# Kernel tuning notes

Measured on AMD Instinct MI355X. Metric: run time of the kernel, lower is better.

## Reference

```python
import jax, jax.numpy as jnp
import numpy as np

M = 32000   # query points
N = 32000   # support points
H = 32      # neighbors per query
C = 64      # channels
K = 15      # kernel points (shell_sizes=[1,14])
GROUPS = 8
CH_PER_GRP = C // GROUPS   # 8
COUT = K * CH_PER_GRP      # 120
RADIUS = 2.5
SIGMA = 1.0
INF = 1.0e6


def _leaky_relu(x):
    return jnp.where(x >= 0, x, 0.1 * x)


def setup_inputs() -> dict:
    key = jax.random.key(0)
    ks = jax.random.split(key, 9)
    q_pts = jax.random.normal(ks[0], (M, 3), jnp.float32) * RADIUS
    s_pts = jax.random.normal(ks[1], (N, 3), jnp.float32) * RADIUS
    s_feats = jax.random.normal(ks[2], (N, C), jnp.float32)
    neighb_inds = jax.random.randint(ks[3], (M, H), 0, N)
    # kernel points in a sphere of given radius, first point fixed at center
    kp = jax.random.normal(ks[4], (K, 3), jnp.float32)
    kp = kp / (jnp.linalg.norm(kp, axis=1, keepdims=True) + 1e-9)
    r = RADIUS * jax.random.uniform(ks[5], (K, 1), jnp.float32) ** (1.0 / 3.0)
    kp = kp * r
    kernel_points = kp.at[0].set(0.0)
    # kaiming-uniform-ish conv weights (K, C)
    bound = 1.0 / np.sqrt(C)
    weights = jax.random.uniform(ks[6], (K, C), jnp.float32, -bound, bound)
    # alpha_mlp: Linear(C,C) + LeakyReLU(0.1) + Linear(C,Cout, no bias)
    w1 = jax.random.normal(ks[7], (C, C), jnp.float32) * (1.0 / np.sqrt(C))
    b1 = jnp.zeros((C,), jnp.float32)
    w2 = jax.random.normal(ks[8], (C, COUT), jnp.float32) * (1.0 / np.sqrt(C))
    return {"q_pts": q_pts, "s_pts": s_pts, "s_feats": s_feats,
            "neighb_inds": neighb_inds, "kernel_points": kernel_points,
            "weights": weights, "w1": w1, "b1": b1, "w2": w2}


def reference(q_pts, s_pts, s_feats, neighb_inds, kernel_points, weights, w1, b1, w2):
    # --- gather neighbor features (padded with a zero row) ---
    padded_feats = jnp.concatenate([s_feats, jnp.zeros((1, C), s_feats.dtype)], axis=0)
    neighbor_feats = padded_feats[neighb_inds]                      # (M, H, C)

    # --- attention modulations (M == N branch: pooled_feats = s_feats) ---
    pooled_feats = s_feats                                           # (M, C)
    mod = _leaky_relu(pooled_feats @ w1 + b1) @ w2                   # (M, Cout)
    mod = jax.nn.sigmoid(mod).reshape(M, K, CH_PER_GRP, 1)
    conv_w = weights.reshape(1, K, CH_PER_GRP, GROUPS) * mod         # (M, K, cpg, g)
    conv_w = conv_w.reshape(M, K, C)

    # --- kernel-point influences (no-grad in original) ---
    s_pts_pad = jnp.concatenate([s_pts, jnp.full((1, 3), INF, s_pts.dtype)], axis=0)
    neighbors = s_pts_pad[neighb_inds] - q_pts[:, None, :]           # (M, H, 3)
    diff = neighbors[:, :, None, :] - kernel_points[None, None, :, :]  # (M, H, K, 3)
    sq_d = jnp.sum(diff * diff, axis=-1)                             # (M, H, K)
    nn_sq = jnp.min(sq_d, axis=2)                                    # (M, H)
    nn_idx = jnp.argmin(sq_d, axis=2)                                # (M, H)
    infl = jnp.clip(1.0 - jnp.sqrt(nn_sq) / SIGMA, 0.0)              # linear influence
    infl = jax.lax.stop_gradient(infl)

    # --- gather per-neighbor kernel weights, modulate and aggregate ---
    nw = jnp.take_along_axis(conv_w, nn_idx[:, :, None], axis=1)     # (M, H, C)
    nw = nw * infl[:, :, None]
    return jnp.sum(neighbor_feats * nw, axis=1)                      # (M, C)
```

## Files before the change

kernel.cpp:

```cpp
#include <hip/hip_runtime.h>


#define MQ 32000

typedef unsigned short u16;
typedef unsigned int   u32;
typedef __attribute__((ext_vector_type(8))) short bf16x8;
typedef __attribute__((ext_vector_type(4))) float f32x4;

__device__ __forceinline__ float rlf(float v, int l) {
    return __int_as_float(__builtin_amdgcn_readlane(__float_as_int(v), l));
}
__device__ __forceinline__ int rli(int v, int l) {
    return __builtin_amdgcn_readlane(v, l);
}
__device__ __forceinline__ u16 f2bf(float x) {
    u32 u = __float_as_uint(x);
    return (u16)((u + 0x7FFFu + ((u >> 16) & 1u)) >> 16);
}
__device__ __forceinline__ float bf2f(u16 b) {
    return __uint_as_float(((u32)b) << 16);
}

__global__ __launch_bounds__(256, 2)
void mod_mlp_mfma(const float* __restrict__ s_feats,
                  const float* __restrict__ w1,
                  const float* __restrict__ b1,
                  const float* __restrict__ w2,
                  float* __restrict__ modw,
                  u16*   __restrict__ fb)
{
    __shared__ u16 w1b[64 * 64];
    __shared__ u16 w2b[64 * 128];
    __shared__ u16 hb[4][16 * 64];

    const int tid = threadIdx.x;
    for (int i = tid; i < 64 * 64; i += 256) w1b[i] = f2bf(w1[i]);
    for (int i = tid; i < 64 * 128; i += 256) {
        int k = i >> 7, j = i & 127;
        w2b[i] = (j < 120) ? f2bf(w2[k * 120 + j]) : (u16)0;
    }
    __syncthreads();

    const int lane = tid & 63;
    const int wid  = tid >> 6;
    const int jj   = lane & 15;
    const int rb   = (lane >> 4) * 8;
    const int rowC = (lane >> 4) * 4;

    bf16x8 b1f[4][2];
    #pragma unroll
    for (int nt = 0; nt < 4; ++nt)
        #pragma unroll
        for (int kk = 0; kk < 2; ++kk)
            #pragma unroll
            for (int r = 0; r < 8; ++r)
                b1f[nt][kk][r] = (short)w1b[(kk * 32 + rb + r) * 64 + nt * 16 + jj];

    bf16x8 b2f[8][2];
    #pragma unroll
    for (int nt = 0; nt < 8; ++nt)
        #pragma unroll
        for (int kk = 0; kk < 2; ++kk)
            #pragma unroll
            for (int r = 0; r < 8; ++r)
                b2f[nt][kk][r] = (short)w2b[(kk * 32 + rb + r) * 128 + nt * 16 + jj];

    float b1v[4];
    #pragma unroll
    for (int nt = 0; nt < 4; ++nt) b1v[nt] = b1[nt * 16 + jj];

    u16* hrow = &hb[wid][0];
    const int t = blockIdx.x * 4 + wid;
    const int m0 = t * 16;

    const float* ar = s_feats + (size_t)(m0 + jj) * 64 + rb;
    float4 v0 = *(const float4*)(ar);
    float4 v1 = *(const float4*)(ar + 4);
    float4 v2 = *(const float4*)(ar + 32);
    float4 v3 = *(const float4*)(ar + 36);
    bf16x8 a0, a1;
    a0[0] = (short)f2bf(v0.x); a0[1] = (short)f2bf(v0.y);
    a0[2] = (short)f2bf(v0.z); a0[3] = (short)f2bf(v0.w);
    a0[4] = (short)f2bf(v1.x); a0[5] = (short)f2bf(v1.y);
    a0[6] = (short)f2bf(v1.z); a0[7] = (short)f2bf(v1.w);
    a1[0] = (short)f2bf(v2.x); a1[1] = (short)f2bf(v2.y);
    a1[2] = (short)f2bf(v2.z); a1[3] = (short)f2bf(v2.w);
    a1[4] = (short)f2bf(v3.x); a1[5] = (short)f2bf(v3.y);
    a1[6] = (short)f2bf(v3.z); a1[7] = (short)f2bf(v3.w);

    *(bf16x8*)(fb + (size_t)(m0 + jj) * 64 + rb)      = a0;
    *(bf16x8*)(fb + (size_t)(m0 + jj) * 64 + 32 + rb) = a1;

    f32x4 acc[4];
    #pragma unroll
    for (int nt = 0; nt < 4; ++nt) {
        f32x4 z = {0.f, 0.f, 0.f, 0.f};
        z = __builtin_amdgcn_mfma_f32_16x16x32_bf16(a0, b1f[nt][0], z, 0, 0, 0);
        acc[nt] = __builtin_amdgcn_mfma_f32_16x16x32_bf16(a1, b1f[nt][1], z, 0, 0, 0);
    }
    #pragma unroll
    for (int nt = 0; nt < 4; ++nt) {
        #pragma unroll
        for (int r = 0; r < 4; ++r) {
            float h = acc[nt][r] + b1v[nt];
            h = (h >= 0.f) ? h : 0.1f * h;
            hrow[(rowC + r) * 64 + nt * 16 + jj] = f2bf(h);
        }
    }
    bf16x8 ha0 = *(bf16x8*)(hrow + jj * 64 + rb);
    bf16x8 ha1 = *(bf16x8*)(hrow + jj * 64 + 32 + rb);

    #pragma unroll
    for (int nt = 0; nt < 8; ++nt) {
        f32x4 z = {0.f, 0.f, 0.f, 0.f};
        z = __builtin_amdgcn_mfma_f32_16x16x32_bf16(ha0, b2f[nt][0], z, 0, 0, 0);
        f32x4 c2 = __builtin_amdgcn_mfma_f32_16x16x32_bf16(ha1, b2f[nt][1], z, 0, 0, 0);
        const int j = nt * 16 + jj;
        if (j < 120) {
            #pragma unroll
            for (int r = 0; r < 4; ++r)
                modw[(size_t)(m0 + rowC + r) * 120 + j] = 1.f / (1.f + __expf(-c2[r]));
        }
    }
}

__global__ __launch_bounds__(256, 4)
void kp_gather_v3(const float* __restrict__ q_pts,
                  const float* __restrict__ s_pts,
                  const u16*   __restrict__ fb,
                  const int*   __restrict__ neighb_inds,
                  const float* __restrict__ kpts,
                  const float* __restrict__ weights,
                  const float* __restrict__ modw,
                  float* __restrict__ out)
{
    __shared__ float wt_lds[15 * 64];
    const int tid = threadIdx.x;
    if (tid < 240) ((float4*)wt_lds)[tid] = ((const float4*)weights)[tid];
    __syncthreads();

    const int lane = tid & 63;
    const int wid  = tid >> 6;
    const int pair = blockIdx.x * 4 + wid;
    const int m0 = pair * 2;

    const int ind = __builtin_nontemporal_load(&neighb_inds[(size_t)m0 * 32 + lane]);

    const int cdiv = lane & 7;
    const int hl   = lane >> 3;
    bf16x8 fv[2][4];
    #pragma unroll
    for (int qq = 0; qq < 2; ++qq)
        #pragma unroll
        for (int cc = 0; cc < 4; ++cc) {
            const int ih = __shfl(ind, qq * 32 + cc * 8 + hl);
            fv[qq][cc] = *(const bf16x8*)(fb + (size_t)(u32)ih * 64 + cdiv * 8);
        }

    const size_t mb0 = (size_t)m0 * 120, mb1 = mb0 + 120;
    const float vA0 = __builtin_nontemporal_load(&modw[mb0 + lane]);
    const float vB0 = (lane < 56) ? __builtin_nontemporal_load(&modw[mb0 + 64 + lane]) : 0.f;
    const float vA1 = __builtin_nontemporal_load(&modw[mb1 + lane]);
    const float vB1 = (lane < 56) ? __builtin_nontemporal_load(&modw[mb1 + 64 + lane]) : 0.f;

    const int q = lane >> 5;
    const int m = m0 + q;
    const float qx = q_pts[m * 3 + 0];
    const float qy = q_pts[m * 3 + 1];
    const float qz = q_pts[m * 3 + 2];
    const float px = s_pts[(size_t)ind * 3 + 0] - qx;
    const float py = s_pts[(size_t)ind * 3 + 1] - qy;
    const float pz = s_pts[(size_t)ind * 3 + 2] - qz;
    float best = 1e30f; int bk = 0;
    #pragma unroll
    for (int k = 0; k < 15; ++k) {
        float ex = px - kpts[k * 3 + 0];
        float ey = py - kpts[k * 3 + 1];
        float ez = pz - kpts[k * 3 + 2];
        float d2 = fmaf(ex, ex, fmaf(ey, ey, ez * ez));
        if (d2 < best) { best = d2; bk = k; }
    }
    const float infl = fmaxf(0.f, 1.f - sqrtf(best));

    float acc[2][8];
    #pragma unroll
    for (int qq = 0; qq < 2; ++qq)
        #pragma unroll
        for (int e = 0; e < 8; ++e) acc[qq][e] = 0.f;

    #pragma unroll
    for (int qq = 0; qq < 2; ++qq) {
        #pragma unroll
        for (int cc = 0; cc < 4; ++cc) {
            const int idx = qq * 32 + cc * 8 + hl;
            const int kh  = __shfl(bk, idx);
            const float fl = __shfl(infl, idx);
            const int j = kh * 8 + cdiv;
            const float svA = __shfl(qq ? vA1 : vA0, j & 63);
            const float svB = __shfl(qq ? vB1 : vB0, (j - 64) & 63);
            const float w = ((j < 64) ? svA : svB) * fl;
            const float4 wa = *(const float4*)&wt_lds[kh * 64 + cdiv * 8];
            const float4 wb = *(const float4*)&wt_lds[kh * 64 + cdiv * 8 + 4];
            const bf16x8 f8 = fv[qq][cc];
            acc[qq][0] = fmaf(bf2f((u16)f8[0]), wa.x * w, acc[qq][0]);
            acc[qq][1] = fmaf(bf2f((u16)f8[1]), wa.y * w, acc[qq][1]);
            acc[qq][2] = fmaf(bf2f((u16)f8[2]), wa.z * w, acc[qq][2]);
            acc[qq][3] = fmaf(bf2f((u16)f8[3]), wa.w * w, acc[qq][3]);
            acc[qq][4] = fmaf(bf2f((u16)f8[4]), wb.x * w, acc[qq][4]);
            acc[qq][5] = fmaf(bf2f((u16)f8[5]), wb.y * w, acc[qq][5]);
            acc[qq][6] = fmaf(bf2f((u16)f8[6]), wb.z * w, acc[qq][6]);
            acc[qq][7] = fmaf(bf2f((u16)f8[7]), wb.w * w, acc[qq][7]);
        }
    }

    #pragma unroll
    for (int step = 8; step <= 32; step <<= 1)
        #pragma unroll
        for (int qq = 0; qq < 2; ++qq)
            #pragma unroll
            for (int e = 0; e < 8; ++e)
                acc[qq][e] += __shfl_xor(acc[qq][e], step);

    if (hl == 0) {
        #pragma unroll
        for (int qq = 0; qq < 2; ++qq) {
            f32x4 o0 = {acc[qq][0], acc[qq][1], acc[qq][2], acc[qq][3]};
            f32x4 o1 = {acc[qq][4], acc[qq][5], acc[qq][6], acc[qq][7]};
            float* dst = out + (size_t)(m0 + qq) * 64 + cdiv * 8;
            __builtin_nontemporal_store(o0, (f32x4*)dst);
            __builtin_nontemporal_store(o1, (f32x4*)(dst + 4));
        }
    }
}

__global__ __launch_bounds__(256, 3)
void mod_mlp(const float* __restrict__ s_feats,
             const float* __restrict__ w1,
             const float* __restrict__ b1,
             const float* __restrict__ w2,
             float* __restrict__ modw)
{
    __shared__ float w1_lds[64 * 64];
    __shared__ float w2_lds[64 * 120 + 8];

    const int tid = threadIdx.x;
    {
        const float4* s1 = (const float4*)w1;
        float4* d1 = (float4*)w1_lds;
        #pragma unroll
        for (int i = 0; i < 4; ++i) d1[tid + 256 * i] = s1[tid + 256 * i];
        const float4* s2 = (const float4*)w2;
        float4* d2 = (float4*)w2_lds;
        for (int i = tid; i < (64 * 120) / 4; i += 256) d2[i] = s2[i];
        if (tid < 8) w2_lds[64 * 120 + tid] = 0.f;
    }
    __syncthreads();

    const int lane = tid & 63;
    const int wid  = tid >> 6;
    const int c    = lane;
    const int nwaves = gridDim.x * 4;
    const int gwave  = blockIdx.x * 4 + wid;
    const float b1v = b1[c];
    const int cB = 64 + ((c < 56) ? c : 55);

    for (int pair = gwave; pair * 2 < MQ; pair += nwaves) {
        const int m0 = pair * 2;
        float f0 = s_feats[(size_t)m0 * 64 + c];
        float f1 = s_feats[(size_t)(m0 + 1) * 64 + c];
        float h0a = b1v, h0b = 0.f, h1a = b1v, h1b = 0.f;
        #pragma unroll
        for (int i = 0; i < 64; i += 2) {
            float wa = w1_lds[i * 64 + c];
            float wb = w1_lds[(i + 1) * 64 + c];
            h0a = fmaf(rlf(f0, i), wa, h0a);
            h0b = fmaf(rlf(f0, i + 1), wb, h0b);
            h1a = fmaf(rlf(f1, i), wa, h1a);
            h1b = fmaf(rlf(f1, i + 1), wb, h1b);
        }
        float h0 = h0a + h0b, h1 = h1a + h1b;
        h0 = (h0 >= 0.f) ? h0 : 0.1f * h0;
        h1 = (h1 >= 0.f) ? h1 : 0.1f * h1;
        float a00 = 0.f, a01 = 0.f, a10 = 0.f, a11 = 0.f;
        #pragma unroll
        for (int i = 0; i < 64; ++i) {
            float wA = w2_lds[i * 120 + c];
            float wB = w2_lds[i * 120 + cB];
            float s0 = rlf(h0, i);
            float s1 = rlf(h1, i);
            a00 = fmaf(s0, wA, a00);
            a01 = fmaf(s0, wB, a01);
            a10 = fmaf(s1, wA, a10);
            a11 = fmaf(s1, wB, a11);
        }
        modw[(size_t)m0 * 120 + c]       = 1.f / (1.f + __expf(-a00));
        modw[(size_t)(m0 + 1) * 120 + c] = 1.f / (1.f + __expf(-a10));
        if (c < 56) {
            modw[(size_t)m0 * 120 + 64 + c]       = 1.f / (1.f + __expf(-a01));
            modw[(size_t)(m0 + 1) * 120 + 64 + c] = 1.f / (1.f + __expf(-a11));
        }
    }
}

__global__ __launch_bounds__(256, 4)
void kp_gather(const float* __restrict__ q_pts,
               const float* __restrict__ s_pts,
               const float* __restrict__ s_feats,
               const int*   __restrict__ neighb_inds,
               const float* __restrict__ kpts,
               const float* __restrict__ weights,
               const float* __restrict__ modw,
               float* __restrict__ out)
{
    __shared__ float wt_lds[15 * 64];
    const int tid = threadIdx.x;
    if (tid < 240) ((float4*)wt_lds)[tid] = ((const float4*)weights)[tid];
    __syncthreads();

    const int lane = tid & 63;
    const int wid  = tid >> 6;
    const int c    = lane;
    const int u    = c >> 3;
    const int pair = blockIdx.x * 4 + wid;
    const int m0 = pair * 2;

    const int q = lane >> 5;
    const int m = m0 + q;
    const int ind = neighb_inds[(size_t)m0 * 32 + lane];
    const float qx = q_pts[m * 3 + 0];
    const float qy = q_pts[m * 3 + 1];
    const float qz = q_pts[m * 3 + 2];
    const float px = s_pts[(size_t)ind * 3 + 0] - qx;
    const float py = s_pts[(size_t)ind * 3 + 1] - qy;
    const float pz = s_pts[(size_t)ind * 3 + 2] - qz;
    float best = 1e30f; int bk = 0;
    #pragma unroll
    for (int k = 0; k < 15; ++k) {
        float ex = px - kpts[k * 3 + 0];
        float ey = py - kpts[k * 3 + 1];
        float ez = pz - kpts[k * 3 + 2];
        float d2 = fmaf(ex, ex, fmaf(ey, ey, ez * ez));
        if (d2 < best) { best = d2; bk = k; }
    }
    const float infl = fmaxf(0.f, 1.f - sqrtf(best));
    const int pk = (ind << 4) | bk;

    const size_t mb0 = (size_t)m0 * 120, mb1 = mb0 + 120;
    const float vA0 = modw[mb0 + c];
    const float vB0 = (c < 56) ? modw[mb0 + 64 + c] : 0.f;
    const float vA1 = modw[mb1 + c];
    const float vB1 = (c < 56) ? modw[mb1 + 64 + c] : 0.f;

    float fv0[32], fv1[32];
    #pragma unroll
    for (int h = 0; h < 32; ++h)
        fv0[h] = s_feats[(size_t)(rli(pk, h) >> 4) * 64 + c];
    #pragma unroll
    for (int h = 0; h < 32; ++h)
        fv1[h] = s_feats[(size_t)(rli(pk, 32 + h) >> 4) * 64 + c];

    float p0 = 0.f, p1 = 0.f, p2 = 0.f, p3 = 0.f;
    #pragma unroll
    for (int h = 0; h < 32; h += 4) {
        #pragma unroll
        for (int j = 0; j < 4; ++j) {
            const int s = rli(pk, h + j);
            const int kh = s & 15;
            const float fl = rlf(infl, h + j);
            const float sv = (kh < 8) ? __shfl(vA0, (kh << 3) + u)
                                      : __shfl(vB0, ((kh - 8) << 3) + u);
            const float w = wt_lds[(kh << 6) + c] * sv * fl;
            float& p = (j == 0) ? p0 : (j == 1) ? p1 : (j == 2) ? p2 : p3;
            p = fmaf(fv0[h + j], w, p);
        }
    }
    const float acc0 = (p0 + p1) + (p2 + p3);

    float r0 = 0.f, r1 = 0.f, r2 = 0.f, r3 = 0.f;
    #pragma unroll
    for (int h = 0; h < 32; h += 4) {
        #pragma unroll
        for (int j = 0; j < 4; ++j) {
            const int s = rli(pk, 32 + h + j);
            const int kh = s & 15;
            const float fl = rlf(infl, 32 + h + j);
            const float sv = (kh < 8) ? __shfl(vA1, (kh << 3) + u)
                                      : __shfl(vB1, ((kh - 8) << 3) + u);
            const float w = wt_lds[(kh << 6) + c] * sv * fl;
            float& p = (j == 0) ? r0 : (j == 1) ? r1 : (j == 2) ? r2 : r3;
            p = fmaf(fv1[h + j], w, p);
        }
    }
    const float acc1 = (r0 + r1) + (r2 + r3);

    out[(size_t)m0 * 64 + c]       = acc0;
    out[(size_t)(m0 + 1) * 64 + c] = acc1;
}

extern "C" void kernel_launch(void* const* d_in, const int* in_sizes, int n_in,
                              void* d_out, int out_size, void* d_ws, size_t ws_size,
                              hipStream_t stream) {
    const float* q_pts       = (const float*)d_in[0];
    const float* s_pts       = (const float*)d_in[1];
    const float* s_feats     = (const float*)d_in[2];
    const int*   neighb_inds = (const int*)d_in[3];
    const float* kpts        = (const float*)d_in[4];
    const float* weights     = (const float*)d_in[5];
    const float* w1          = (const float*)d_in[6];
    const float* b1          = (const float*)d_in[7];
    const float* w2          = (const float*)d_in[8];
    float* out = (float*)d_out;

    const size_t needFB   = (size_t)MQ * 64 * sizeof(u16);
    const size_t needMODW = (size_t)MQ * 120 * sizeof(float);
    if (ws_size >= needFB + needMODW) {
        u16*   fb   = (u16*)d_ws;
        float* modw = (float*)((char*)d_ws + needFB);
        mod_mlp_mfma<<<500, 256, 0, stream>>>(s_feats, w1, b1, w2, modw, fb);
        kp_gather_v3<<<MQ / 8, 256, 0, stream>>>(q_pts, s_pts, fb, neighb_inds,
                                                 kpts, weights, modw, out);
    } else {
        float* modw = (float*)d_ws;
        mod_mlp<<<768, 256, 0, stream>>>(s_feats, w1, b1, w2, modw);
        kp_gather<<<MQ / 8, 256, 0, stream>>>(q_pts, s_pts, s_feats, neighb_inds,
                                              kpts, weights, modw, out);
    }
}
```

Measured before the change: 116.9 us.

## Store modulation weights as bf16 and pre-pack MLP weight fragments in a prep kernel

Adds a one-block prep kernel that converts w1/w2 to bf16 in MFMA fragment order, so each MLP block loads its B fragments directly instead of converting through LDS with a barrier. The sigmoid modulation tensor is written as bf16 and read as packed 32-bit pairs in the gather kernel, halving that intermediate's write and read traffic. This costs an extra kernel launch and lowers modulation precision to bf16.

```diff
diff --git a/kernel.cpp b/kernel.cpp
--- a/kernel.cpp
+++ b/kernel.cpp
@@ -22,56 +22,45 @@
     return __uint_as_float(((u32)b) << 16);
 }
 
+__global__ void prep_weights(const float* __restrict__ w1,
+                             const float* __restrict__ w2,
+                             u16* __restrict__ w1p,
+                             u16* __restrict__ w2p)
+{
+    const int tid = threadIdx.x;
+    for (int i = tid; i < 64 * 64; i += 256) {
+        const int k = i >> 6, j = i & 63;
+        const int dst = (((k >> 5) * 4 + ((k >> 3) & 3)) * 4 + (j >> 4)) * 128
+                        + (j & 15) * 8 + (k & 7);
+        w1p[dst] = f2bf(w1[i]);
+    }
+    for (int i = tid; i < 64 * 128; i += 256) {
+        const int k = i >> 7, j = i & 127;
+        const int dst = (((k >> 5) * 4 + ((k >> 3) & 3)) * 8 + (j >> 4)) * 128
+                        + (j & 15) * 8 + (k & 7);
+        w2p[dst] = (j < 120) ? f2bf(w2[k * 120 + j]) : (u16)0;
+    }
+}
+
 __global__ __launch_bounds__(256, 2)
-void mod_mlp_mfma(const float* __restrict__ s_feats,
-                  const float* __restrict__ w1,
-                  const float* __restrict__ b1,
-                  const float* __restrict__ w2,
-                  float* __restrict__ modw,
-                  u16*   __restrict__ fb)
+void mod_mlp_mfma2(const float* __restrict__ s_feats,
+                   const u16*   __restrict__ w1p,
+                   const float* __restrict__ b1,
+                   const u16*   __restrict__ w2p,
+                   u16* __restrict__ modw,
+                   u16* __restrict__ fb)
 {
-    __shared__ u16 w1b[64 * 64];
-    __shared__ u16 w2b[64 * 128];
     __shared__ u16 hb[4][16 * 64];
 
-    const int tid = threadIdx.x;
-    for (int i = tid; i < 64 * 64; i += 256) w1b[i] = f2bf(w1[i]);
-    for (int i = tid; i < 64 * 128; i += 256) {
-        int k = i >> 7, j = i & 127;
-        w2b[i] = (j < 120) ? f2bf(w2[k * 120 + j]) : (u16)0;
-    }
-    __syncthreads();
-
+    const int tid  = threadIdx.x;
     const int lane = tid & 63;
     const int wid  = tid >> 6;
     const int jj   = lane & 15;
-    const int rb   = (lane >> 4) * 8;
-    const int rowC = (lane >> 4) * 4;
-
-    bf16x8 b1f[4][2];
-    #pragma unroll
-    for (int nt = 0; nt < 4; ++nt)
-        #pragma unroll
-        for (int kk = 0; kk < 2; ++kk)
-            #pragma unroll
-            for (int r = 0; r < 8; ++r)
-                b1f[nt][kk][r] = (short)w1b[(kk * 32 + rb + r) * 64 + nt * 16 + jj];
-
-    bf16x8 b2f[8][2];
-    #pragma unroll
-    for (int nt = 0; nt < 8; ++nt)
-        #pragma unroll
-        for (int kk = 0; kk < 2; ++kk)
-            #pragma unroll
-            for (int r = 0; r < 8; ++r)
-                b2f[nt][kk][r] = (short)w2b[(kk * 32 + rb + r) * 128 + nt * 16 + jj];
-
-    float b1v[4];
-    #pragma unroll
-    for (int nt = 0; nt < 4; ++nt) b1v[nt] = b1[nt * 16 + jj];
-
-    u16* hrow = &hb[wid][0];
-    const int t = blockIdx.x * 4 + wid;
+    const int rbg  = lane >> 4;
+    const int rb   = rbg * 8;
+    const int rowC = rbg * 4;
+
+    const int t  = blockIdx.x * 4 + wid;
     const int m0 = t * 16;
 
     const float* ar = s_feats + (size_t)(m0 + jj) * 64 + rb;
@@ -92,13 +81,20 @@
     *(bf16x8*)(fb + (size_t)(m0 + jj) * 64 + rb)      = a0;
     *(bf16x8*)(fb + (size_t)(m0 + jj) * 64 + 32 + rb) = a1;
 
+    float b1v[4];
+    #pragma unroll
+    for (int nt = 0; nt < 4; ++nt) b1v[nt] = b1[nt * 16 + jj];
+
     f32x4 acc[4];
     #pragma unroll
     for (int nt = 0; nt < 4; ++nt) {
+        const bf16x8 f0 = *(const bf16x8*)(w1p + ((0 * 4 + rbg) * 4 + nt) * 128 + jj * 8);
+        const bf16x8 f1 = *(const bf16x8*)(w1p + ((1 * 4 + rbg) * 4 + nt) * 128 + jj * 8);
         f32x4 z = {0.f, 0.f, 0.f, 0.f};
-        z = __builtin_amdgcn_mfma_f32_16x16x32_bf16(a0, b1f[nt][0], z, 0, 0, 0);
-        acc[nt] = __builtin_amdgcn_mfma_f32_16x16x32_bf16(a1, b1f[nt][1], z, 0, 0, 0);
-    }
+        z = __builtin_amdgcn_mfma_f32_16x16x32_bf16(a0, f0, z, 0, 0, 0);
+        acc[nt] = __builtin_amdgcn_mfma_f32_16x16x32_bf16(a1, f1, z, 0, 0, 0);
+    }
+    u16* hrow = &hb[wid][0];
     #pragma unroll
     for (int nt = 0; nt < 4; ++nt) {
         #pragma unroll
@@ -108,31 +104,34 @@
             hrow[(rowC + r) * 64 + nt * 16 + jj] = f2bf(h);
         }
     }
-    bf16x8 ha0 = *(bf16x8*)(hrow + jj * 64 + rb);
-    bf16x8 ha1 = *(bf16x8*)(hrow + jj * 64 + 32 + rb);
+    const bf16x8 ha0 = *(bf16x8*)(hrow + jj * 64 + rb);
+    const bf16x8 ha1 = *(bf16x8*)(hrow + jj * 64 + 32 + rb);
 
     #pragma unroll
     for (int nt = 0; nt < 8; ++nt) {
+        const bf16x8 g0 = *(const bf16x8*)(w2p + ((0 * 4 + rbg) * 8 + nt) * 128 + jj * 8);
+        const bf16x8 g1 = *(const bf16x8*)(w2p + ((1 * 4 + rbg) * 8 + nt) * 128 + jj * 8);
         f32x4 z = {0.f, 0.f, 0.f, 0.f};
-        z = __builtin_amdgcn_mfma_f32_16x16x32_bf16(ha0, b2f[nt][0], z, 0, 0, 0);
-        f32x4 c2 = __builtin_amdgcn_mfma_f32_16x16x32_bf16(ha1, b2f[nt][1], z, 0, 0, 0);
+        z = __builtin_amdgcn_mfma_f32_16x16x32_bf16(ha0, g0, z, 0, 0, 0);
+        f32x4 c2 = __builtin_amdgcn_mfma_f32_16x16x32_bf16(ha1, g1, z, 0, 0, 0);
         const int j = nt * 16 + jj;
         if (j < 120) {
             #pragma unroll
             for (int r = 0; r < 4; ++r)
-                modw[(size_t)(m0 + rowC + r) * 120 + j] = 1.f / (1.f + __expf(-c2[r]));
+                modw[(size_t)(m0 + rowC + r) * 120 + j] =
+                    f2bf(1.f / (1.f + __expf(-c2[r])));
         }
     }
 }
 
 __global__ __launch_bounds__(256, 4)
-void kp_gather_v3(const float* __restrict__ q_pts,
+void kp_gather_v4(const float* __restrict__ q_pts,
                   const float* __restrict__ s_pts,
                   const u16*   __restrict__ fb,
                   const int*   __restrict__ neighb_inds,
                   const float* __restrict__ kpts,
                   const float* __restrict__ weights,
-                  const float* __restrict__ modw,
+                  const u32*   __restrict__ modw32,
                   float* __restrict__ out)
 {
     __shared__ float wt_lds[15 * 64];
@@ -158,11 +157,8 @@
             fv[qq][cc] = *(const bf16x8*)(fb + (size_t)(u32)ih * 64 + cdiv * 8);
         }
 
-    const size_t mb0 = (size_t)m0 * 120, mb1 = mb0 + 120;
-    const float vA0 = __builtin_nontemporal_load(&modw[mb0 + lane]);
-    const float vB0 = (lane < 56) ? __builtin_nontemporal_load(&modw[mb0 + 64 + lane]) : 0.f;
-    const float vA1 = __builtin_nontemporal_load(&modw[mb1 + lane]);
-    const float vB1 = (lane < 56) ? __builtin_nontemporal_load(&modw[mb1 + 64 + lane]) : 0.f;
+    const u32 W0 = (lane < 60) ? __builtin_nontemporal_load(&modw32[(size_t)m0 * 60 + lane]) : 0u;
+    const u32 W1 = (lane < 60) ? __builtin_nontemporal_load(&modw32[(size_t)(m0 + 1) * 60 + lane]) : 0u;
 
     const int q = lane >> 5;
     const int m = m0 + q;
@@ -197,9 +193,9 @@
             const int kh  = __shfl(bk, idx);
             const float fl = __shfl(infl, idx);
             const int j = kh * 8 + cdiv;
-            const float svA = __shfl(qq ? vA1 : vA0, j & 63);
-            const float svB = __shfl(qq ? vB1 : vB0, (j - 64) & 63);
-            const float w = ((j < 64) ? svA : svB) * fl;
+            const u32 w32 = (u32)__shfl((int)(qq ? W1 : W0), j >> 1);
+            const u16 hbf = (j & 1) ? (u16)(w32 >> 16) : (u16)(w32 & 0xffffu);
+            const float w = bf2f(hbf) * fl;
             const float4 wa = *(const float4*)&wt_lds[kh * 64 + cdiv * 8];
             const float4 wb = *(const float4*)&wt_lds[kh * 64 + cdiv * 8 + 4];
             const bf16x8 f8 = fv[qq][cc];
@@ -412,15 +408,23 @@
     const float* w2          = (const float*)d_in[8];
     float* out = (float*)d_out;
 
-    const size_t needFB   = (size_t)MQ * 64 * sizeof(u16);
-    const size_t needMODW = (size_t)MQ * 120 * sizeof(float);
-    if (ws_size >= needFB + needMODW) {
-        u16*   fb   = (u16*)d_ws;
-        float* modw = (float*)((char*)d_ws + needFB);
-        mod_mlp_mfma<<<500, 256, 0, stream>>>(s_feats, w1, b1, w2, modw, fb);
-        kp_gather_v3<<<MQ / 8, 256, 0, stream>>>(q_pts, s_pts, fb, neighb_inds,
-                                                 kpts, weights, modw, out);
-    } else {
+    const size_t offFB   = 0;
+    const size_t offMODW = (size_t)MQ * 64 * sizeof(u16);
+    const size_t offW1P  = offMODW + (size_t)MQ * 120 * sizeof(u16);
+    const size_t offW2P  = offW1P + 4096 * sizeof(u16);
+    const size_t needBF  = offW2P + 8192 * sizeof(u16);
+    const size_t needF32 = (size_t)MQ * 120 * sizeof(float);
+
+    if (ws_size >= needBF) {
+        u16* fb    = (u16*)((char*)d_ws + offFB);
+        u16* modwb = (u16*)((char*)d_ws + offMODW);
+        u16* w1p   = (u16*)((char*)d_ws + offW1P);
+        u16* w2p   = (u16*)((char*)d_ws + offW2P);
+        prep_weights<<<1, 256, 0, stream>>>(w1, w2, w1p, w2p);
+        mod_mlp_mfma2<<<500, 256, 0, stream>>>(s_feats, w1p, b1, w2p, modwb, fb);
+        kp_gather_v4<<<MQ / 8, 256, 0, stream>>>(q_pts, s_pts, fb, neighb_inds,
+                                                 kpts, weights, (const u32*)modwb, out);
+    } else if (ws_size >= needF32) {
         float* modw = (float*)d_ws;
         mod_mlp<<<768, 256, 0, stream>>>(s_feats, w1, b1, w2, modw);
         kp_gather<<<MQ / 8, 256, 0, stream>>>(q_pts, s_pts, s_feats, neighb_inds,
```

New measurement: 120.2 us. +2.8%, slower.
